# Kernel optimization log

Measured on AMD Instinct MI355X. Metric: run time of the kernel, lower is better.

Reference implementation:

```python
import jax, jax.numpy as jnp
from jax import lax
import numpy as np

GROUPS = 4


def _grid_sample_border(img, gx, gy):
    # img: [Bg, Cg, H, W]; gx, gy: [Bg, H, W] normalized grid in [-1, 1]
    # Replicates F.grid_sample(mode='bilinear', align_corners=False, padding_mode='border')
    Bg, Cg, H, W = img.shape
    ix = jnp.clip(((gx + 1.0) * W - 1.0) * 0.5, 0.0, W - 1.0)
    iy = jnp.clip(((gy + 1.0) * H - 1.0) * 0.5, 0.0, H - 1.0)
    x0 = jnp.floor(ix)
    y0 = jnp.floor(iy)
    wx = ix - x0
    wy = iy - y0
    x0i = x0.astype(jnp.int32)
    y0i = y0.astype(jnp.int32)
    x1i = jnp.minimum(x0i + 1, W - 1)
    y1i = jnp.minimum(y0i + 1, H - 1)

    def one(im, x0i, x1i, y0i, y1i, wx, wy):
        v00 = im[:, y0i, x0i]
        v01 = im[:, y0i, x1i]
        v10 = im[:, y1i, x0i]
        v11 = im[:, y1i, x1i]
        return (v00 * (1 - wx) * (1 - wy) + v01 * wx * (1 - wy)
                + v10 * (1 - wx) * wy + v11 * wx * wy)

    return jax.vmap(one)(img, x0i, x1i, y0i, y1i, wx, wy)


def setup_inputs() -> dict:
    key = jax.random.key(0)
    ks = jax.random.split(key, 8)
    B, N, C = 8, 4096, 768
    x = jax.random.normal(ks[0], (B, N, C), dtype=jnp.float32)
    dw_w = jax.random.normal(ks[1], (C, 1, 3, 3), dtype=jnp.float32) * 0.1  # depthwise kernel
    dw_b = jax.random.normal(ks[2], (C,), dtype=jnp.float32) * 0.1
    off_w = jax.random.normal(ks[3], (2 * GROUPS, C), dtype=jnp.float32) * 0.001  # std=0.001 init
    off_b = jnp.zeros((2 * GROUPS,), dtype=jnp.float32)
    wt_w = jax.random.normal(ks[4], (2 * GROUPS, C), dtype=jnp.float32) * 0.02
    wt_b = jnp.zeros((2 * GROUPS,), dtype=jnp.float32)
    offset_list = jnp.zeros((1,), dtype=jnp.int32)
    return {"x": x, "dw_w": dw_w, "dw_b": dw_b, "off_w": off_w, "off_b": off_b,
            "wt_w": wt_w, "wt_b": wt_b, "offset_list": offset_list,
            "patch_h": 64, "patch_w": 64}


def reference(x, dw_w, dw_b, off_w, off_b, wt_w, wt_b, offset_list, patch_h, patch_w):
    B, N, C = x.shape
    H, W = int(patch_h), int(patch_w)
    xi = jnp.transpose(x, (0, 2, 1)).reshape(B, C, H, W)

    # offset head: depthwise 3x3 conv -> GELU -> 1x1 conv to 2*groups channels
    dw = lax.conv_general_dilated(xi, dw_w, (1, 1), ((1, 1), (1, 1)),
                                  dimension_numbers=("NCHW", "OIHW", "NCHW"),
                                  feature_group_count=C)
    dw = jax.nn.gelu(dw + dw_b[None, :, None, None], approximate=False)
    off = jnp.einsum("bchw,oc->bohw", dw, off_w) + off_b[None, :, None, None]

    # weight head: 1x1 conv -> sigmoid
    wt = jax.nn.sigmoid(jnp.einsum("bchw,oc->bohw", xi, wt_w) + wt_b[None, :, None, None])

    off = (off * wt).reshape(B, 2, GROUPS, H, W)
    # fixed cross-shaped shifts: x-comp [0,0,-1,+1], y-comp [-1,+1,0,0]
    shifts = jnp.array([[0.0, 0.0, -1.0, 1.0], [-1.0, 1.0, 0.0, 0.0]],
                       dtype=x.dtype).reshape(1, 2, GROUPS, 1, 1)
    off = off + shifts

    cx = (jnp.arange(W, dtype=x.dtype) + 0.5)[None, None, None, :]  # pixel-center x coords
    cy = (jnp.arange(H, dtype=x.dtype) + 0.5)[None, None, :, None]  # pixel-center y coords
    gx = 2.0 * (cx + off[:, 0]) / W - 1.0  # [B, GROUPS, H, W]
    gy = 2.0 * (cy + off[:, 1]) / H - 1.0

    img = xi.reshape(B * GROUPS, C // GROUPS, H, W)
    samp = _grid_sample_border(img, gx.reshape(B * GROUPS, H, W),
                               gy.reshape(B * GROUPS, H, W))
    out = samp.reshape(B, C, N)
    return jnp.transpose(out, (0, 2, 1))  # [B, N, C]
```

## Files before the change

### kernel.cpp

```cpp
#include <hip/hip_runtime.h>
#include <math.h>

#define BB 8
#define CC 768
#define HH 64
#define WW 64
#define NN 4096
#define GG 4
#define NCHUNK 6
#define CHUNK 128

typedef __attribute__((ext_vector_type(8))) short short8;
typedef __attribute__((ext_vector_type(4))) float f32x4;

__device__ __forceinline__ unsigned short f2bf(float f) {
    union { float f; unsigned u; } v; v.f = f;
    unsigned r = v.u + 0x7FFFu + ((v.u >> 16) & 1u);
    return (unsigned short)(r >> 16);
}

__device__ __forceinline__ float gelu_fast(float v) {
    const float z = 1.5957691216f * v * fmaf(0.044715f, v * v, 1.0f);
    return __fdividef(v, 1.0f + __expf(-z));
}

__global__ __launch_bounds__(128, 4) void dq_conv_mfma(
    const float* __restrict__ x,
    const float* __restrict__ dw_w,
    const float* __restrict__ dw_b,
    const float* __restrict__ off_w,
    const float* __restrict__ wt_w,
    float* __restrict__ offpart)
{
    __shared__ unsigned short gl[32][136];
    __shared__ unsigned short xh[32][136];
    const int t = threadIdx.x;
    const int lane = t & 63, wv = t >> 6;
    int bid = blockIdx.x;
    const int chunk = bid % NCHUNK; bid /= NCHUNK;
    const int h = bid % HH;
    const int b = bid / HH;
    const int c = chunk * CHUNK + t;

    const int n = lane & 15, kg = lane >> 4;
    short8 bfrag[8];
#pragma unroll
    for (int kt = 0; kt < 8; ++kt) {
        const bool isOff = (kt < 4);
        const bool valid = isOff ? (n < 8) : (n >= 8);
        const int krow = isOff ? kt : kt - 4;
        const float* wp = isOff ? (off_w + (n < 8 ? n : 0) * CC)
                                : (wt_w + (n >= 8 ? n - 8 : 0) * CC);
        const float* src = wp + chunk * CHUNK + krow * 32 + kg * 8;
        short8 bf;
#pragma unroll
        for (int j = 0; j < 8; ++j) {
            const float v = valid ? src[j] : 0.f;
            bf[j] = (short)f2bf(v);
        }
        bfrag[kt] = bf;
    }

    float w9[9];
#pragma unroll
    for (int j = 0; j < 9; ++j) w9[j] = dw_w[c * 9 + j];
    const float bias = dw_b[c];
    const bool tv = (h > 0), bv = (h < HH - 1);
    const float wt0 = tv ? w9[0] : 0.f, wt1 = tv ? w9[1] : 0.f, wt2 = tv ? w9[2] : 0.f;
    const float wb0 = bv ? w9[6] : 0.f, wb1 = bv ? w9[7] : 0.f, wb2 = bv ? w9[8] : 0.f;

    const float* base = x + (size_t)b * NN * CC + c;
    const float* rT = base + (size_t)((tv ? h - 1 : 0) * WW) * CC;
    const float* rM = base + (size_t)(h * WW) * CC;
    const float* rB = base + (size_t)((bv ? h + 1 : h) * WW) * CC;

    float cT[8], cM[8], cB[8], nT[8], nM[8], nB[8];
    float pT = 0.f, pM = 0.f, pB = 0.f;

#pragma unroll
    for (int j = 0; j < 8; ++j) {
        const size_t o = (size_t)j * CC;
        cT[j] = rT[o]; cM[j] = rM[o]; cB[j] = rB[o];
    }

    for (int wb = 0; wb < 8; ++wb) {
        if (wb < 7) {
#pragma unroll
            for (int j = 0; j < 8; ++j) {
                const size_t o = (size_t)(wb * 8 + 8 + j) * CC;
                nT[j] = rT[o]; nM[j] = rM[o]; nB[j] = rB[o];
            }
        } else {
#pragma unroll
            for (int j = 0; j < 8; ++j) { nT[j] = 0.f; nM[j] = 0.f; nB[j] = 0.f; }
        }
#pragma unroll
        for (int j = 0; j < 8; ++j) {
            const float lT = j ? cT[j - 1] : pT;
            const float lM = j ? cM[j - 1] : pM;
            const float lB = j ? cB[j - 1] : pB;
            const float rTv = (j == 7) ? nT[0] : cT[j + 1];
            const float rMv = (j == 7) ? nM[0] : cM[j + 1];
            const float rBv = (j == 7) ? nB[0] : cB[j + 1];
            const float conv = lT * wt0 + cT[j] * wt1 + rTv * wt2
                             + lM * w9[3] + cM[j] * w9[4] + rMv * w9[5]
                             + lB * wb0 + cB[j] * wb1 + rBv * wb2;
            const int colh = (wb & 3) * 8 + j;
            gl[colh][t] = f2bf(gelu_fast(conv + bias));
            xh[colh][t] = f2bf(cM[j]);
        }
        pT = cT[7]; pM = cM[7]; pB = cB[7];
#pragma unroll
        for (int j = 0; j < 8; ++j) { cT[j] = nT[j]; cM[j] = nM[j]; cB[j] = nB[j]; }

        if ((wb & 3) == 3) {
            const int half = wb >> 2;
            __syncthreads();
            f32x4 acc = {0.f, 0.f, 0.f, 0.f};
            const int arow = wv * 16 + n;
#pragma unroll
            for (int kt = 0; kt < 4; ++kt) {
                const short8 a = *(const short8*)&gl[arow][kt * 32 + kg * 8];
                acc = __builtin_amdgcn_mfma_f32_16x16x32_bf16(a, bfrag[kt], acc, 0, 0, 0);
            }
#pragma unroll
            for (int kt = 0; kt < 4; ++kt) {
                const short8 a = *(const short8*)&xh[arow][kt * 32 + kg * 8];
                acc = __builtin_amdgcn_mfma_f32_16x16x32_bf16(a, bfrag[4 + kt], acc, 0, 0, 0);
            }
            const size_t gpos = (size_t)(b * NN) + h * WW + half * 32 + wv * 16 + kg * 4;
            float4 st; st.x = acc[0]; st.y = acc[1]; st.z = acc[2]; st.w = acc[3];
            *(float4*)&offpart[((size_t)(chunk * 16 + n)) * (BB * NN) + gpos] = st;
            if (wb < 7) __syncthreads();
        }
    }
}

__global__ __launch_bounds__(256) void dq_combine(
    const float* __restrict__ offpart,
    const float* __restrict__ off_b,
    const float* __restrict__ wt_b,
    float* __restrict__ ixiy)
{
    const int t = threadIdx.x;
    const int o = t >> 5;
    const int gpos = blockIdx.x * 32 + (t & 31);
    const int b = gpos >> 12;
    const int hw = gpos & 4095;
    const int h = hw >> 6, w = hw & 63;

    float so = 0.f, sw = 0.f;
#pragma unroll
    for (int ch = 0; ch < NCHUNK; ++ch) {
        so += offpart[((size_t)(ch * 16 + o)) * (BB * NN) + gpos];
        sw += offpart[((size_t)(ch * 16 + 8 + o)) * (BB * NN) + gpos];
    }
    const float sig = 1.f / (1.f + __expf(-(sw + wt_b[o])));
    const float val = (so + off_b[o]) * sig;

    if (o < 4) {
        const float shx = (o == 2) ? -1.f : ((o == 3) ? 1.f : 0.f);
        const float ix = fminf(fmaxf((float)w + val + shx, 0.f), (float)(WW - 1));
        ixiy[(b * GG + o) * NN + hw] = ix;
    } else {
        const int g = o - 4;
        const float shy = (g == 0) ? -1.f : ((g == 1) ? 1.f : 0.f);
        const float iy = fminf(fmaxf((float)h + val + shy, 0.f), (float)(HH - 1));
        ixiy[BB * GG * NN + (b * GG + g) * NN + hw] = iy;
    }
}

__global__ __launch_bounds__(192) void dq_sample_vec(
    const float* __restrict__ x,
    const float* __restrict__ ixiy,
    float* __restrict__ out)
{
    __shared__ float ixy[8];
    const int t = threadIdx.x;
    const int p = (blockIdx.x & 7) * (BB * NN / 8) + (blockIdx.x >> 3);
    const int b = p >> 12;
    const int hw = p & 4095;

    if (t < 8) {
        const int g = t & 3;
        const int plane = (t >> 2) * (BB * GG * NN);
        ixy[t] = ixiy[plane + (b * GG + g) * NN + hw];
    }
    __syncthreads();

    const int g = t / 48;
    const float ix = ixy[g], iy = ixy[4 + g];
    const float x0f = floorf(ix), y0f = floorf(iy);
    const float wx = ix - x0f, wy = iy - y0f;
    const int x0 = (int)x0f, y0 = (int)y0f;
    const int x1 = min(x0 + 1, WW - 1), y1 = min(y0 + 1, HH - 1);
    const int c4 = t * 4;
    const float* xb = x + (size_t)b * NN * CC;
    const float4 v00 = *(const float4*)(xb + (size_t)(y0 * WW + x0) * CC + c4);
    const float4 v01 = *(const float4*)(xb + (size_t)(y0 * WW + x1) * CC + c4);
    const float4 v10 = *(const float4*)(xb + (size_t)(y1 * WW + x0) * CC + c4);
    const float4 v11 = *(const float4*)(xb + (size_t)(y1 * WW + x1) * CC + c4);
    const float w00 = (1.f - wx) * (1.f - wy), w01 = wx * (1.f - wy);
    const float w10 = (1.f - wx) * wy,         w11 = wx * wy;
    float4 r;
    r.x = v00.x * w00 + v01.x * w01 + v10.x * w10 + v11.x * w11;
    r.y = v00.y * w00 + v01.y * w01 + v10.y * w10 + v11.y * w11;
    r.z = v00.z * w00 + v01.z * w01 + v10.z * w10 + v11.z * w11;
    r.w = v00.w * w00 + v01.w * w01 + v10.w * w10 + v11.w * w11;
    *(float4*)(out + (size_t)p * CC + c4) = r;
}

__global__ __launch_bounds__(256) void dqshift_offsets_kernel(
    const float* __restrict__ x, const float* __restrict__ dw_w,
    const float* __restrict__ dw_b, const float* __restrict__ off_w,
    const float* __restrict__ off_b, const float* __restrict__ wt_w,
    const float* __restrict__ wt_b, float* __restrict__ ixiy)
{
    const int wave = threadIdx.x >> 6;
    const int lane = threadIdx.x & 63;
    const int p = blockIdx.x * 4 + wave;
    const int b = p >> 12;
    const int hw = p & 4095;
    const int h = hw >> 6;
    const int w = hw & 63;
    const float* xb = x + (size_t)b * NN * CC;
    float accO[8], accW[8];
#pragma unroll
    for (int o = 0; o < 8; ++o) { accO[o] = 0.f; accW[o] = 0.f; }
    for (int k = 0; k < CC / 64; ++k) {
        const int c = lane + (k << 6);
        float conv = 0.f, xc = 0.f;
#pragma unroll
        for (int dy = -1; dy <= 1; ++dy) {
            const int hh = h + dy;
            const bool vy = (hh >= 0) && (hh < HH);
#pragma unroll
            for (int dx = -1; dx <= 1; ++dx) {
                const int ww = w + dx;
                const bool vv = vy && (ww >= 0) && (ww < WW);
                const float tt = vv ? xb[(size_t)(hh * WW + ww) * CC + c] : 0.f;
                if (dy == 0 && dx == 0) xc = tt;
                conv = fmaf(tt, dw_w[c * 9 + (dy + 1) * 3 + (dx + 1)], conv);
            }
        }
        const float gv = conv + dw_b[c];
        const float gle = 0.5f * gv * (1.0f + erff(gv * 0.70710678118654752f));
#pragma unroll
        for (int o = 0; o < 8; ++o) {
            accO[o] = fmaf(gle, off_w[o * CC + c], accO[o]);
            accW[o] = fmaf(xc, wt_w[o * CC + c], accW[o]);
        }
    }
#pragma unroll
    for (int o = 0; o < 8; ++o) {
#pragma unroll
        for (int s = 32; s > 0; s >>= 1) {
            accO[o] += __shfl_xor(accO[o], s, 64);
            accW[o] += __shfl_xor(accW[o], s, 64);
        }
    }
    if (lane == 0) {
        const float shx[4] = {0.f, 0.f, -1.f, 1.f};
        const float shy[4] = {-1.f, 1.f, 0.f, 0.f};
#pragma unroll
        for (int g = 0; g < 4; ++g) {
            const float sx = 1.f / (1.f + expf(-(accW[g] + wt_b[g])));
            const float sy = 1.f / (1.f + expf(-(accW[4 + g] + wt_b[4 + g])));
            const float ox = (accO[g] + off_b[g]) * sx + shx[g];
            const float oy = (accO[4 + g] + off_b[4 + g]) * sy + shy[g];
            const float ix = fminf(fmaxf((float)w + ox, 0.f), (float)(WW - 1));
            const float iy = fminf(fmaxf((float)h + oy, 0.f), (float)(HH - 1));
            const int idx = (b * GG + g) * NN + hw;
            ixiy[idx] = ix;
            ixiy[BB * GG * NN + idx] = iy;
        }
    }
}

__global__ __launch_bounds__(256) void dqshift_sample_kernel(
    const float* __restrict__ x,
    const float* __restrict__ ixiy,
    float* __restrict__ out)
{
    const int p = blockIdx.x;
    const int b = p >> 12;
    const int hw = p & 4095;
    const float* xb = x + (size_t)b * NN * CC;
    float* ob = out + (size_t)p * CC;

#pragma unroll
    for (int k = 0; k < 3; ++k) {
        const int c = threadIdx.x + (k << 8);
        const int g = c / (CC / GG);
        const int idx = (b * GG + g) * NN + hw;
        const float ix = ixiy[idx];
        const float iy = ixiy[BB * GG * NN + idx];
        const float x0f = floorf(ix);
        const float y0f = floorf(iy);
        const float wx = ix - x0f;
        const float wy = iy - y0f;
        const int x0 = (int)x0f;
        const int y0 = (int)y0f;
        const int x1 = min(x0 + 1, WW - 1);
        const int y1 = min(y0 + 1, HH - 1);
        const float* r0 = xb + (size_t)(y0 * WW) * CC + c;
        const float* r1 = xb + (size_t)(y1 * WW) * CC + c;
        const float v00 = r0[(size_t)x0 * CC];
        const float v01 = r0[(size_t)x1 * CC];
        const float v10 = r1[(size_t)x0 * CC];
        const float v11 = r1[(size_t)x1 * CC];
        ob[c] = v00 * (1.f - wx) * (1.f - wy) + v01 * wx * (1.f - wy)
              + v10 * (1.f - wx) * wy + v11 * wx * wy;
    }
}

extern "C" void kernel_launch(void* const* d_in, const int* in_sizes, int n_in,
                              void* d_out, int out_size, void* d_ws, size_t ws_size,
                              hipStream_t stream) {
    const float* x     = (const float*)d_in[0];
    const float* dw_w  = (const float*)d_in[1];
    const float* dw_b  = (const float*)d_in[2];
    const float* off_w = (const float*)d_in[3];
    const float* off_b = (const float*)d_in[4];
    const float* wt_w  = (const float*)d_in[5];
    const float* wt_b  = (const float*)d_in[6];

    float* ixiy = (float*)d_ws;
    float* offpart = (float*)d_ws + 2 * BB * GG * NN;
    const size_t need = (size_t)(2 * BB * GG * NN + NCHUNK * 16 * BB * NN) * 4;

    if (ws_size >= need) {
        dq_conv_mfma<<<BB * HH * NCHUNK, 128, 0, stream>>>(
            x, dw_w, dw_b, off_w, wt_w, offpart);
        dq_combine<<<BB * NN / 32, 256, 0, stream>>>(
            offpart, off_b, wt_b, ixiy);
        dq_sample_vec<<<BB * NN, 192, 0, stream>>>(
            x, ixiy, (float*)d_out);
    } else {
        dqshift_offsets_kernel<<<BB * NN / 4, 256, 0, stream>>>(
            x, dw_w, dw_b, off_w, off_b, wt_w, wt_b, ixiy);
        dqshift_sample_kernel<<<BB * NN, 256, 0, stream>>>(x, ixiy, (float*)d_out);
    }
}
```

Measured before the change: 92.51 us.

## Split offset and weight-head MFMAs across waves with smaller LDS staging

The conv kernel now has wave 0 compute the offset-head projection from GELU values and wave 1 compute the weight-head projection from raw x. Before, each wave did both projections against zero-padded B fragments. This halves the B fragments held per lane (8 to 4) and shrinks the LDS tiles from 32 to 16 columns, flushing every 16 columns instead of every 32. The catch is twice as many barriers and MFMA rounds per block, and only half the lanes store results.

```diff
diff --git a/kernel.cpp b/kernel.cpp
--- a/kernel.cpp
+++ b/kernel.cpp
@@ -32,8 +32,8 @@
     const float* __restrict__ wt_w,
     float* __restrict__ offpart)
 {
-    __shared__ unsigned short gl[32][136];
-    __shared__ unsigned short xh[32][136];
+    __shared__ unsigned short gl[16][144];
+    __shared__ unsigned short xh[16][144];
     const int t = threadIdx.x;
     const int lane = t & 63, wv = t >> 6;
     int bid = blockIdx.x;
@@ -43,15 +43,12 @@
     const int c = chunk * CHUNK + t;
 
     const int n = lane & 15, kg = lane >> 4;
-    short8 bfrag[8];
-#pragma unroll
-    for (int kt = 0; kt < 8; ++kt) {
-        const bool isOff = (kt < 4);
-        const bool valid = isOff ? (n < 8) : (n >= 8);
-        const int krow = isOff ? kt : kt - 4;
-        const float* wp = isOff ? (off_w + (n < 8 ? n : 0) * CC)
-                                : (wt_w + (n >= 8 ? n - 8 : 0) * CC);
-        const float* src = wp + chunk * CHUNK + krow * 32 + kg * 8;
+    const float* wsrc = (wv == 0) ? off_w : wt_w;
+    short8 bfrag[4];
+#pragma unroll
+    for (int kt = 0; kt < 4; ++kt) {
+        const bool valid = (n < 8);
+        const float* src = wsrc + (valid ? n : 0) * CC + chunk * CHUNK + kt * 32 + kg * 8;
         short8 bf;
 #pragma unroll
         for (int j = 0; j < 8; ++j) {
@@ -83,56 +80,63 @@
         cT[j] = rT[o]; cM[j] = rM[o]; cB[j] = rB[o];
     }
 
-    for (int wb = 0; wb < 8; ++wb) {
-        if (wb < 7) {
+#pragma unroll
+    for (int q = 0; q < 4; ++q) {
+#pragma unroll
+        for (int hb = 0; hb < 2; ++hb) {
+            const int wb = q * 2 + hb;
+            if (wb < 7) {
+#pragma unroll
+                for (int j = 0; j < 8; ++j) {
+                    const size_t o = (size_t)(wb * 8 + 8 + j) * CC;
+                    nT[j] = rT[o]; nM[j] = rM[o]; nB[j] = rB[o];
+                }
+            } else {
+#pragma unroll
+                for (int j = 0; j < 8; ++j) { nT[j] = 0.f; nM[j] = 0.f; nB[j] = 0.f; }
+            }
 #pragma unroll
             for (int j = 0; j < 8; ++j) {
-                const size_t o = (size_t)(wb * 8 + 8 + j) * CC;
-                nT[j] = rT[o]; nM[j] = rM[o]; nB[j] = rB[o];
+                const float lT = j ? cT[j - 1] : pT;
+                const float lM = j ? cM[j - 1] : pM;
+                const float lB = j ? cB[j - 1] : pB;
+                const float rTv = (j == 7) ? nT[0] : cT[j + 1];
+                const float rMv = (j == 7) ? nM[0] : cM[j + 1];
+                const float rBv = (j == 7) ? nB[0] : cB[j + 1];
+                const float conv = lT * wt0 + cT[j] * wt1 + rTv * wt2
+                                 + lM * w9[3] + cM[j] * w9[4] + rMv * w9[5]
+                                 + lB * wb0 + cB[j] * wb1 + rBv * wb2;
+                const int colq = hb * 8 + j;
+                gl[colq][t] = f2bf(gelu_fast(conv + bias));
+                xh[colq][t] = f2bf(cM[j]);
+            }
+            pT = cT[7]; pM = cM[7]; pB = cB[7];
+#pragma unroll
+            for (int j = 0; j < 8; ++j) { cT[j] = nT[j]; cM[j] = nM[j]; cB[j] = nB[j]; }
+        }
+
+        __syncthreads();
+        f32x4 acc = {0.f, 0.f, 0.f, 0.f};
+        if (wv == 0) {
+#pragma unroll
+            for (int kt = 0; kt < 4; ++kt) {
+                const short8 a = *(const short8*)&gl[n][kt * 32 + kg * 8];
+                acc = __builtin_amdgcn_mfma_f32_16x16x32_bf16(a, bfrag[kt], acc, 0, 0, 0);
             }
         } else {
 #pragma unroll
-            for (int j = 0; j < 8; ++j) { nT[j] = 0.f; nM[j] = 0.f; nB[j] = 0.f; }
-        }
-#pragma unroll
-        for (int j = 0; j < 8; ++j) {
-            const float lT = j ? cT[j - 1] : pT;
-            const float lM = j ? cM[j - 1] : pM;
-            const float lB = j ? cB[j - 1] : pB;
-            const float rTv = (j == 7) ? nT[0] : cT[j + 1];
-            const float rMv = (j == 7) ? nM[0] : cM[j + 1];
-            const float rBv = (j == 7) ? nB[0] : cB[j + 1];
-            const float conv = lT * wt0 + cT[j] * wt1 + rTv * wt2
-                             + lM * w9[3] + cM[j] * w9[4] + rMv * w9[5]
-                             + lB * wb0 + cB[j] * wb1 + rBv * wb2;
-            const int colh = (wb & 3) * 8 + j;
-            gl[colh][t] = f2bf(gelu_fast(conv + bias));
-            xh[colh][t] = f2bf(cM[j]);
-        }
-        pT = cT[7]; pM = cM[7]; pB = cB[7];
-#pragma unroll
-        for (int j = 0; j < 8; ++j) { cT[j] = nT[j]; cM[j] = nM[j]; cB[j] = nB[j]; }
-
-        if ((wb & 3) == 3) {
-            const int half = wb >> 2;
-            __syncthreads();
-            f32x4 acc = {0.f, 0.f, 0.f, 0.f};
-            const int arow = wv * 16 + n;
-#pragma unroll
             for (int kt = 0; kt < 4; ++kt) {
-                const short8 a = *(const short8*)&gl[arow][kt * 32 + kg * 8];
+                const short8 a = *(const short8*)&xh[n][kt * 32 + kg * 8];
                 acc = __builtin_amdgcn_mfma_f32_16x16x32_bf16(a, bfrag[kt], acc, 0, 0, 0);
             }
-#pragma unroll
-            for (int kt = 0; kt < 4; ++kt) {
-                const short8 a = *(const short8*)&xh[arow][kt * 32 + kg * 8];
-                acc = __builtin_amdgcn_mfma_f32_16x16x32_bf16(a, bfrag[4 + kt], acc, 0, 0, 0);
-            }
-            const size_t gpos = (size_t)(b * NN) + h * WW + half * 32 + wv * 16 + kg * 4;
+        }
+        if (n < 8) {
+            const int plane = chunk * 16 + (wv ? 8 + n : n);
+            const size_t gpos = (size_t)(b * NN) + h * WW + q * 16 + kg * 4;
             float4 st; st.x = acc[0]; st.y = acc[1]; st.z = acc[2]; st.w = acc[3];
-            *(float4*)&offpart[((size_t)(chunk * 16 + n)) * (BB * NN) + gpos] = st;
-            if (wb < 7) __syncthreads();
-        }
+            *(float4*)&offpart[(size_t)plane * (BB * NN) + gpos] = st;
+        }
+        if (q < 3) __syncthreads();
     }
 }
 
```

New measurement: 87.47 us. 1.06x faster.
